# Performance work log

Measured on AMD Instinct MI355X. Metric: run time of the kernel, lower is better.

The kernel has to match this reference:

```python
import jax, jax.numpy as jnp
import numpy as np

D_MODEL = 512
D_PROJ = 32
N_CENT = 6
CORR_HIDDEN = max(D_MODEL // 16, 32)  # 32
LN_EPS = 1e-5
ALPHA_DIR = 5.0


def _layernorm(x, g, b):
    mu = x.mean(axis=-1, keepdims=True)
    var = jnp.mean((x - mu) ** 2, axis=-1, keepdims=True)
    return (x - mu) * jax.lax.rsqrt(var + LN_EPS) * g + b


def _l2norm(x, eps=1e-12):
    n = jnp.sqrt(jnp.sum(x * x, axis=-1, keepdims=True))
    return x / jnp.maximum(n, eps)


def setup_inputs() -> dict:
    key = jax.random.key(0)
    ks = jax.random.split(key, 8)
    B, N = 64, 1024
    x = jax.random.normal(ks[0], (B, N, D_MODEL), dtype=jnp.float32)
    s_in = 1.0 / np.sqrt(D_MODEL)
    proj_w = jax.random.uniform(ks[1], (D_PROJ, D_MODEL), jnp.float32, -s_in, s_in)
    proj_b = jax.random.uniform(ks[2], (D_PROJ,), jnp.float32, -s_in, s_in)
    ln_g = jnp.ones((D_PROJ,), jnp.float32)
    ln_b = jnp.zeros((D_PROJ,), jnp.float32)
    centroids = jax.random.uniform(ks[3], (N_CENT, D_PROJ), jnp.float32, -3.0, 3.0)
    s_c = 1.0 / np.sqrt(D_MODEL + D_PROJ)
    corr_in_w = jax.random.uniform(ks[4], (CORR_HIDDEN, D_MODEL + D_PROJ), jnp.float32, -s_c, s_c)
    corr_in_b = jax.random.uniform(ks[5], (CORR_HIDDEN,), jnp.float32, -s_c, s_c)
    # correction_out is zero-init in the module; use small random values so the
    # correction path is numerically exercised by the baseline.
    corr_out_w = jax.random.normal(ks[6], (D_MODEL, CORR_HIDDEN), jnp.float32) * 0.02
    corr_out_b = jax.random.normal(ks[7], (D_MODEL,), jnp.float32) * 0.02
    return {
        "x": x, "proj_w": proj_w, "proj_b": proj_b, "ln_g": ln_g, "ln_b": ln_b,
        "centroids": centroids,
        "corr_in_w": corr_in_w, "corr_in_b": corr_in_b,
        "corr_out_w": corr_out_w, "corr_out_b": corr_out_b,
        "gate_alpha": jnp.float32(0.0),
        "routing_log_temp": jnp.float32(1.6),
        "scale_evidence": jnp.float32(5.0),
    }


def reference(x, proj_w, proj_b, ln_g, ln_b, centroids, corr_in_w, corr_in_b,
              corr_out_w, corr_out_b, gate_alpha, routing_log_temp, scale_evidence):
    B, N, D = x.shape
    # per-variate RevIN-style normalization over the variate axis (dim=1), unbiased std
    rev_mean = x.mean(axis=1, keepdims=True)
    rev_var = jnp.sum((x - rev_mean) ** 2, axis=1, keepdims=True) / (N - 1)
    rev_std = jnp.sqrt(rev_var) + 1e-5
    x_norm = (x - rev_mean) / rev_std
    # geometric routing: proj -> LN -> cosine sim against centroids
    Q = _layernorm(jnp.einsum("bnd,pd->bnp", x_norm, proj_w) + proj_b, ln_g, ln_b)
    Q_n = _l2norm(Q)                      # [B,N,P]
    K_n = _l2norm(centroids)              # [K,P]
    sim_cos = jnp.einsum("bnp,kp->bnk", Q_n, K_n)
    soft_assign = jax.nn.softmax(sim_cos * jnp.exp(routing_log_temp), axis=-1)
    centroid_ctx = jnp.einsum("bnk,kp->bnp", soft_assign, centroids)
    # centroid-conditioned correction MLP (dropout is identity in eval)
    corr_input = jnp.concatenate([x_norm, centroid_ctx], axis=-1)  # [B,N,D+P]
    h = jax.nn.gelu(jnp.einsum("bnc,hc->bnh", corr_input, corr_in_w) + corr_in_b, approximate=False)
    correction = (jnp.einsum("bnh,dh->bnd", h, corr_out_w) + corr_out_b) * rev_std
    gate = jax.nn.sigmoid(gate_alpha)
    out = x + gate * correction
    # DST uncertainty (no-grad diagnostic)
    sim_ctrl = jax.lax.stop_gradient(sim_cos)
    dir_gate = jax.nn.softplus((sim_ctrl - sim_ctrl.mean(axis=-1, keepdims=True)) * ALPHA_DIR)
    s_ev = jax.nn.softplus(jax.lax.stop_gradient(scale_evidence))
    S_train = jnp.sum(dir_gate * s_ev + 1.0, axis=-1, keepdims=True)
    u_std = N_CENT / S_train
    # losses
    gram = K_n @ K_n.T
    ortho_loss = jnp.mean((gram - jnp.eye(N_CENT, dtype=x.dtype)) ** 2)
    avg_routing = soft_assign.mean(axis=(0, 1))
    latent_loss = jnp.mean((avg_routing - 1.0 / N_CENT) ** 2)
    return out, u_std, ortho_loss, latent_loss
```

## Files before the change

kernel.cpp:

```cpp
#include <hip/hip_runtime.h>
#include <cstdint>
#include <cstddef>

#define N_DIM 1024
#define D_DIM 512
#define M_DIM 65536
#define NC 6

typedef float f32x4 __attribute__((ext_vector_type(4)));
typedef __bf16 bf16x8 __attribute__((ext_vector_type(8)));

__device__ __forceinline__ float sp_f(float z) {
    return z > 20.f ? z : log1pf(expf(z));
}

__global__ void k_ortho(const float* __restrict__ cent, float* __restrict__ out_ortho) {
    __shared__ float skn[NC * 32];
    __shared__ float ssq[36];
    int t = threadIdx.x;
    if (t < NC) {
        float s = 0.f;
        for (int p = 0; p < 32; ++p) { float v = cent[t * 32 + p]; s += v * v; }
        float inv = 1.f / fmaxf(sqrtf(s), 1e-12f);
        for (int p = 0; p < 32; ++p) skn[t * 32 + p] = cent[t * 32 + p] * inv;
    }
    __syncthreads();
    if (t < 36) {
        int i = t / 6, j = t % 6;
        float g = 0.f;
        for (int p = 0; p < 32; ++p) g += skn[i * 32 + p] * skn[j * 32 + p];
        float d = g - (i == j ? 1.f : 0.f);
        ssq[t] = d * d;
    }
    __syncthreads();
    if (t == 0) {
        float s = 0.f;
        for (int i = 0; i < 36; ++i) s += ssq[i];
        *out_ortho = s / 36.f;
    }
}

__global__ void k_stat1(const float* __restrict__ x, float* __restrict__ part) {
    int bid = blockIdx.x;
    int b = bid >> 3, c = bid & 7;
    int d = threadIdx.x;
    const float* px = x + ((size_t)(b * N_DIM + c * 128)) * D_DIM + d;
    float s = 0.f, q = 0.f;
    for (int i = 0; i < 128; ++i) {
        float v = px[(size_t)i * D_DIM];
        s += v; q += v * v;
    }
    size_t o = ((size_t)bid * D_DIM + d) * 2;
    part[o] = s;
    part[o + 1] = q;
}

__global__ void k_stat2(const float* __restrict__ part, float* __restrict__ mean,
                        float* __restrict__ istd) {
    int b = blockIdx.x, d = threadIdx.x;
    float s = 0.f, q = 0.f;
    for (int c = 0; c < 8; ++c) {
        size_t o = (((size_t)(b * 8 + c)) * D_DIM + d) * 2;
        s += part[o]; q += part[o + 1];
    }
    float mu = s * (1.f / (float)N_DIM);
    float var = fmaxf((q - s * mu) * (1.f / (float)(N_DIM - 1)), 0.f);
    float sd = sqrtf(var) + 1e-5f;
    mean[b * D_DIM + d] = mu;
    istd[b * D_DIM + d] = 1.f / sd;
}

__launch_bounds__(256)
__global__ void mega(const float* __restrict__ x,
                     const float* __restrict__ pw, const float* __restrict__ proj_b,
                     const float* __restrict__ ln_g, const float* __restrict__ ln_b,
                     const float* __restrict__ cent,
                     const float* __restrict__ ciw, const float* __restrict__ cib,
                     const float* __restrict__ cow, const float* __restrict__ cob,
                     const float* __restrict__ ga, const float* __restrict__ rlt,
                     const float* __restrict__ sev,
                     const float* __restrict__ mean, const float* __restrict__ istd,
                     float* __restrict__ out, float* __restrict__ ustd_out,
                     float* __restrict__ acc_rout) {
    __shared__ float s_tile[4][16][65];
    __shared__ __align__(16) __bf16 s_h[4][16][40];
    __shared__ float s_asg[64][6];
    __shared__ float s_kn[192], s_cw[192];
    __shared__ float s_pb[32], s_g[32], s_bl[32], s_b2[32];
    __shared__ float s_scal[3];

    int tid = threadIdx.x;
    int wv = tid >> 6, ln = tid & 63;
    int l15 = ln & 15, lg = ln >> 4;

    if (tid < 192) {
        int k = tid >> 5, h = tid & 31;
        float s = 0.f;
        for (int p = 0; p < 32; ++p) s += cent[k * 32 + p] * ciw[h * 544 + 512 + p];
        s_cw[k * 32 + h] = s;
    }
    if (tid >= 192 && tid < 192 + NC) {
        int k = tid - 192;
        float s = 0.f;
        for (int p = 0; p < 32; ++p) { float v = cent[k * 32 + p]; s += v * v; }
        float inv = 1.f / fmaxf(sqrtf(s), 1e-12f);
        for (int p = 0; p < 32; ++p) s_kn[k * 32 + p] = cent[k * 32 + p] * inv;
    }
    if (tid == 198) {
        s_scal[0] = expf(rlt[0]);
        s_scal[1] = sp_f(sev[0]);
        s_scal[2] = 1.f / (1.f + expf(-ga[0]));
    }
    if (tid < 32) s_pb[tid] = proj_b[tid];
    else if (tid < 64) s_g[tid - 32] = ln_g[tid - 32];
    else if (tid < 96) s_bl[tid - 64] = ln_b[tid - 64];
    else if (tid < 128) s_b2[tid - 96] = cib[tid - 96];
    __syncthreads();

    int row0 = blockIdx.x * 64;
    int b = row0 >> 10;
    int wrow = row0 + wv * 16;
    int myrow = wrow + l15;

    const float* xr = x + (size_t)myrow * D_DIM;
    const float* mb = mean + b * D_DIM;
    const float* ib = istd + b * D_DIM;

    const float* wrow_[4];
    wrow_[0] = pw + (size_t)l15 * 512;
    wrow_[1] = pw + (size_t)(16 + l15) * 512;
    wrow_[2] = ciw + (size_t)l15 * 544;
    wrow_[3] = ciw + (size_t)(16 + l15) * 544;

    f32x4 acc[4];
    #pragma unroll
    for (int nf = 0; nf < 4; ++nf) acc[nf] = (f32x4){0.f, 0.f, 0.f, 0.f};

    for (int ks = 0; ks < 16; ++ks) {
        int k0 = ks * 32 + lg * 8;
        float4 xa = *(const float4*)(xr + k0);
        float4 xb = *(const float4*)(xr + k0 + 4);
        float4 ma = *(const float4*)(mb + k0);
        float4 m2 = *(const float4*)(mb + k0 + 4);
        float4 ia = *(const float4*)(ib + k0);
        float4 i2 = *(const float4*)(ib + k0 + 4);
        float xnf[8];
        xnf[0] = (xa.x - ma.x) * ia.x; xnf[1] = (xa.y - ma.y) * ia.y;
        xnf[2] = (xa.z - ma.z) * ia.z; xnf[3] = (xa.w - ma.w) * ia.w;
        xnf[4] = (xb.x - m2.x) * i2.x; xnf[5] = (xb.y - m2.y) * i2.y;
        xnf[6] = (xb.z - m2.z) * i2.z; xnf[7] = (xb.w - m2.w) * i2.w;
        bf16x8 ah, al;
        #pragma unroll
        for (int j = 0; j < 8; ++j) {
            __bf16 h = (__bf16)xnf[j];
            ah[j] = h;
            al[j] = (__bf16)(xnf[j] - (float)h);
        }
        #pragma unroll
        for (int nf = 0; nf < 4; ++nf) {
            float4 wa = *(const float4*)(wrow_[nf] + k0);
            float4 wb4 = *(const float4*)(wrow_[nf] + k0 + 4);
            float wf[8];
            wf[0] = wa.x; wf[1] = wa.y; wf[2] = wa.z; wf[3] = wa.w;
            wf[4] = wb4.x; wf[5] = wb4.y; wf[6] = wb4.z; wf[7] = wb4.w;
            bf16x8 wh;
            #pragma unroll
            for (int j = 0; j < 8; ++j) wh[j] = (__bf16)wf[j];
            acc[nf] = __builtin_amdgcn_mfma_f32_16x16x32_bf16(ah, wh, acc[nf], 0, 0, 0);
            if (nf < 2) {
                bf16x8 wl;
                #pragma unroll
                for (int j = 0; j < 8; ++j) wl[j] = (__bf16)(wf[j] - (float)wh[j]);
                acc[nf] = __builtin_amdgcn_mfma_f32_16x16x32_bf16(ah, wl, acc[nf], 0, 0, 0);
                acc[nf] = __builtin_amdgcn_mfma_f32_16x16x32_bf16(al, wh, acc[nf], 0, 0, 0);
            }
        }
    }
    #pragma unroll
    for (int nf = 0; nf < 4; ++nf)
        #pragma unroll
        for (int rg = 0; rg < 4; ++rg)
            s_tile[wv][lg * 4 + rg][nf * 16 + l15] = acc[nf][rg];
    __syncthreads();

    if (ln < 16) {
        int r = ln;
        int grow = wrow + r;
        const float* trow = &s_tile[wv][r][0];
        float P[32]; float mu = 0.f;
        #pragma unroll
        for (int p = 0; p < 32; ++p) { P[p] = trow[p] + s_pb[p]; mu += P[p]; }
        mu *= (1.f / 32.f);
        float var = 0.f;
        #pragma unroll
        for (int p = 0; p < 32; ++p) { float d = P[p] - mu; var += d * d; }
        var *= (1.f / 32.f);
        float rs = rsqrtf(var + 1e-5f);
        float q[32]; float n2 = 0.f;
        #pragma unroll
        for (int p = 0; p < 32; ++p) {
            q[p] = (P[p] - mu) * rs * s_g[p] + s_bl[p];
            n2 += q[p] * q[p];
        }
        float inv = 1.f / fmaxf(sqrtf(n2), 1e-12f);
        float sim[6];
        #pragma unroll
        for (int k = 0; k < 6; ++k) {
            float s = 0.f;
            #pragma unroll
            for (int p = 0; p < 32; ++p) s += q[p] * s_kn[k * 32 + p];
            sim[k] = s * inv;
        }
        float T = s_scal[0];
        float mx = sim[0];
        #pragma unroll
        for (int k = 1; k < 6; ++k) mx = fmaxf(mx, sim[k]);
        float e[6], es = 0.f;
        #pragma unroll
        for (int k = 0; k < 6; ++k) { e[k] = expf((sim[k] - mx) * T); es += e[k]; }
        float einv = 1.f / es;
        float a[6];
        #pragma unroll
        for (int k = 0; k < 6; ++k) { a[k] = e[k] * einv; s_asg[wv * 16 + r][k] = a[k]; }
        float msim = 0.f;
        #pragma unroll
        for (int k = 0; k < 6; ++k) msim += sim[k];
        msim *= (1.f / 6.f);
        float S = 6.f, sevv = s_scal[1];
        #pragma unroll
        for (int k = 0; k < 6; ++k) S += sevv * sp_f((sim[k] - msim) * 5.f);
        ustd_out[grow] = 6.f / S;
        #pragma unroll
        for (int h = 0; h < 32; ++h) {
            float v = trow[32 + h] + s_b2[h];
            #pragma unroll
            for (int k = 0; k < 6; ++k) v += a[k] * s_cw[k * 32 + h];
            float g = 0.5f * v * (1.f + erff(v * 0.70710678118654752f));
            s_h[wv][r][h] = (__bf16)g;
        }
    }
    __syncthreads();

    bf16x8 ha = *(const bf16x8*)&s_h[wv][l15][lg * 8];
    float gate = s_scal[2];
    for (int nf = 0; nf < 32; ++nf) {
        int col = nf * 16 + l15;
        float4 wa = *(const float4*)(cow + (size_t)col * 32 + lg * 8);
        float4 wb4 = *(const float4*)(cow + (size_t)col * 32 + lg * 8 + 4);
        bf16x8 wb;
        wb[0] = (__bf16)wa.x; wb[1] = (__bf16)wa.y; wb[2] = (__bf16)wa.z; wb[3] = (__bf16)wa.w;
        wb[4] = (__bf16)wb4.x; wb[5] = (__bf16)wb4.y; wb[6] = (__bf16)wb4.z; wb[7] = (__bf16)wb4.w;
        f32x4 z = (f32x4){0.f, 0.f, 0.f, 0.f};
        f32x4 d = __builtin_amdgcn_mfma_f32_16x16x32_bf16(ha, wb, z, 0, 0, 0);
        float bias = cob[col];
        float rsd = 1.f / ib[col];
        #pragma unroll
        for (int rg = 0; rg < 4; ++rg) {
            int row = wrow + lg * 4 + rg;
            float xv = x[(size_t)row * D_DIM + col];
            out[(size_t)row * D_DIM + col] = xv + gate * ((d[rg] + bias) * rsd);
        }
    }

    if (tid < 6) {
        float s = 0.f;
        for (int r = 0; r < 64; ++r) s += s_asg[r][tid];
        atomicAdd(acc_rout + tid, s);
    }
}

__global__ void k5(const float* __restrict__ acc, float* __restrict__ out_latent) {
    if (threadIdx.x == 0) {
        float s = 0.f;
        for (int k = 0; k < 6; ++k) {
            float av = acc[k] * (1.f / (float)M_DIM);
            float d = av - (1.f / 6.f);
            s += d * d;
        }
        *out_latent = s / 6.f;
    }
}

extern "C" void kernel_launch(void* const* d_in, const int* in_sizes, int n_in,
                              void* d_out, int out_size, void* d_ws, size_t ws_size,
                              hipStream_t stream) {
    const float* x      = (const float*)d_in[0];
    const float* proj_w = (const float*)d_in[1];
    const float* proj_b = (const float*)d_in[2];
    const float* ln_g   = (const float*)d_in[3];
    const float* ln_b   = (const float*)d_in[4];
    const float* cent   = (const float*)d_in[5];
    const float* ciw    = (const float*)d_in[6];
    const float* cib    = (const float*)d_in[7];
    const float* cow    = (const float*)d_in[8];
    const float* cob    = (const float*)d_in[9];
    const float* ga     = (const float*)d_in[10];
    const float* rlt    = (const float*)d_in[11];
    const float* sev    = (const float*)d_in[12];

    char* ws = (char*)d_ws;
    float* acc  = (float*)(ws + 0);
    float* mean = (float*)(ws + 1024);
    float* istd = (float*)(ws + 1024 + 131072);

    float* outp   = (float*)d_out;
    float* ustd   = outp + (size_t)M_DIM * D_DIM;
    float* ortho  = ustd + M_DIM;
    float* latent = ortho + 1;

    float* part = (float*)d_out;

    hipMemsetAsync(acc, 0, 6 * sizeof(float), stream);
    k_ortho<<<1, 64, 0, stream>>>(cent, ortho);
    k_stat1<<<512, 512, 0, stream>>>(x, part);
    k_stat2<<<64, 512, 0, stream>>>(part, mean, istd);
    mega<<<1024, 256, 0, stream>>>(x, proj_w, proj_b, ln_g, ln_b, cent, ciw, cib,
                                   cow, cob, ga, rlt, sev, mean, istd,
                                   outp, ustd, acc);
    k5<<<1, 64, 0, stream>>>(acc, latent);
}
```

Measured before the change: 174.3 us.

## Prepack weights to bf16 in a separate kernel and parallelize per-row epilogue

Adds a k_pack kernel that converts projection and correction weights to bf16 hi/lo splits once and precomputes normalized centroids, centroid-correction products and scalars, so the mega kernel no longer reconverts weights and recomputes these per block. The per-row LayerNorm/routing/GELU epilogue is spread across 4 lanes per row with shuffles instead of 16 lanes doing everything serially. The block barriers are dropped because each wave only touches its own smem slice. Routing sums go into 64 partial slots to reduce atomic contention, and a precomputed std replaces the per-column reciprocal. The cost is an extra kernel launch and more workspace traffic.

```diff
diff --git a/kernel.cpp b/kernel.cpp
--- a/kernel.cpp
+++ b/kernel.cpp
@@ -12,6 +12,45 @@
 
 __device__ __forceinline__ float sp_f(float z) {
     return z > 20.f ? z : log1pf(expf(z));
+}
+
+__global__ void k_pack(const float* __restrict__ pw, const float* __restrict__ ciw,
+                       const float* __restrict__ cow, const float* __restrict__ cent,
+                       const float* __restrict__ ga, const float* __restrict__ rlt,
+                       const float* __restrict__ sev,
+                       __bf16* __restrict__ bpa, __bf16* __restrict__ bpl,
+                       __bf16* __restrict__ w3p,
+                       float* __restrict__ kn, float* __restrict__ cw,
+                       float* __restrict__ scal) {
+    int bid = blockIdx.x, tid = threadIdx.x;
+    if (bid < 128) {
+        int i = bid * 256 + tid;
+        int c = i >> 9, k = i & 511;
+        float w = (c < 32) ? pw[c * 512 + k] : ciw[(c - 32) * 544 + k];
+        __bf16 hi = (__bf16)w;
+        bpa[i] = hi;
+        if (c < 32) bpl[i] = (__bf16)(w - (float)hi);
+    } else if (bid < 192) {
+        int j = (bid - 128) * 256 + tid;
+        w3p[j] = (__bf16)cow[j];
+    } else {
+        if (tid < 192) {
+            int k = tid >> 5, h = tid & 31;
+            float s = 0.f;
+            for (int p = 0; p < 32; ++p) s += cent[k * 32 + p] * ciw[h * 544 + 512 + p];
+            cw[k * 32 + h] = s;
+        } else if (tid < 192 + NC) {
+            int k = tid - 192;
+            float s = 0.f;
+            for (int p = 0; p < 32; ++p) { float v = cent[k * 32 + p]; s += v * v; }
+            float inv = 1.f / fmaxf(sqrtf(s), 1e-12f);
+            for (int p = 0; p < 32; ++p) kn[k * 32 + p] = cent[k * 32 + p] * inv;
+        } else if (tid == 198) {
+            scal[0] = expf(rlt[0]);
+            scal[1] = sp_f(sev[0]);
+            scal[2] = 1.f / (1.f + expf(-ga[0]));
+        }
+    }
 }
 
 __global__ void k_ortho(const float* __restrict__ cent, float* __restrict__ out_ortho) {
@@ -56,7 +95,7 @@
 }
 
 __global__ void k_stat2(const float* __restrict__ part, float* __restrict__ mean,
-                        float* __restrict__ istd) {
+                        float* __restrict__ istd, float* __restrict__ stdv) {
     int b = blockIdx.x, d = threadIdx.x;
     float s = 0.f, q = 0.f;
     for (int c = 0; c < 8; ++c) {
@@ -68,74 +107,46 @@
     float sd = sqrtf(var) + 1e-5f;
     mean[b * D_DIM + d] = mu;
     istd[b * D_DIM + d] = 1.f / sd;
+    stdv[b * D_DIM + d] = sd;
 }
 
 __launch_bounds__(256)
 __global__ void mega(const float* __restrict__ x,
-                     const float* __restrict__ pw, const float* __restrict__ proj_b,
-                     const float* __restrict__ ln_g, const float* __restrict__ ln_b,
-                     const float* __restrict__ cent,
-                     const float* __restrict__ ciw, const float* __restrict__ cib,
-                     const float* __restrict__ cow, const float* __restrict__ cob,
-                     const float* __restrict__ ga, const float* __restrict__ rlt,
-                     const float* __restrict__ sev,
+                     const float* __restrict__ proj_b, const float* __restrict__ ln_g,
+                     const float* __restrict__ ln_b, const float* __restrict__ cib,
+                     const float* __restrict__ cob,
                      const float* __restrict__ mean, const float* __restrict__ istd,
+                     const float* __restrict__ stdv,
+                     const float* __restrict__ kn, const float* __restrict__ cw,
+                     const float* __restrict__ scal,
+                     const __bf16* __restrict__ bpa, const __bf16* __restrict__ bpl,
+                     const __bf16* __restrict__ w3p,
                      float* __restrict__ out, float* __restrict__ ustd_out,
-                     float* __restrict__ acc_rout) {
-    __shared__ float s_tile[4][16][65];
+                     float* __restrict__ rout_part) {
+    __shared__ __align__(16) float s_tile[4][16][68];
     __shared__ __align__(16) __bf16 s_h[4][16][40];
-    __shared__ float s_asg[64][6];
-    __shared__ float s_kn[192], s_cw[192];
-    __shared__ float s_pb[32], s_g[32], s_bl[32], s_b2[32];
-    __shared__ float s_scal[3];
 
     int tid = threadIdx.x;
     int wv = tid >> 6, ln = tid & 63;
     int l15 = ln & 15, lg = ln >> 4;
 
-    if (tid < 192) {
-        int k = tid >> 5, h = tid & 31;
-        float s = 0.f;
-        for (int p = 0; p < 32; ++p) s += cent[k * 32 + p] * ciw[h * 544 + 512 + p];
-        s_cw[k * 32 + h] = s;
-    }
-    if (tid >= 192 && tid < 192 + NC) {
-        int k = tid - 192;
-        float s = 0.f;
-        for (int p = 0; p < 32; ++p) { float v = cent[k * 32 + p]; s += v * v; }
-        float inv = 1.f / fmaxf(sqrtf(s), 1e-12f);
-        for (int p = 0; p < 32; ++p) s_kn[k * 32 + p] = cent[k * 32 + p] * inv;
-    }
-    if (tid == 198) {
-        s_scal[0] = expf(rlt[0]);
-        s_scal[1] = sp_f(sev[0]);
-        s_scal[2] = 1.f / (1.f + expf(-ga[0]));
-    }
-    if (tid < 32) s_pb[tid] = proj_b[tid];
-    else if (tid < 64) s_g[tid - 32] = ln_g[tid - 32];
-    else if (tid < 96) s_bl[tid - 64] = ln_b[tid - 64];
-    else if (tid < 128) s_b2[tid - 96] = cib[tid - 96];
-    __syncthreads();
-
     int row0 = blockIdx.x * 64;
     int b = row0 >> 10;
     int wrow = row0 + wv * 16;
-    int myrow = wrow + l15;
-
-    const float* xr = x + (size_t)myrow * D_DIM;
+
+    const float* xr = x + (size_t)(wrow + l15) * D_DIM;
     const float* mb = mean + b * D_DIM;
     const float* ib = istd + b * D_DIM;
 
-    const float* wrow_[4];
-    wrow_[0] = pw + (size_t)l15 * 512;
-    wrow_[1] = pw + (size_t)(16 + l15) * 512;
-    wrow_[2] = ciw + (size_t)l15 * 544;
-    wrow_[3] = ciw + (size_t)(16 + l15) * 544;
-
-    f32x4 acc[4];
-    #pragma unroll
-    for (int nf = 0; nf < 4; ++nf) acc[nf] = (f32x4){0.f, 0.f, 0.f, 0.f};
-
+    const __bf16* w0 = bpa + (size_t)l15 * 512;
+    const __bf16* w1 = bpa + (size_t)(16 + l15) * 512;
+    const __bf16* w2 = bpa + (size_t)(32 + l15) * 512;
+    const __bf16* w3 = bpa + (size_t)(48 + l15) * 512;
+    const __bf16* wl0 = bpl + (size_t)l15 * 512;
+    const __bf16* wl1 = bpl + (size_t)(16 + l15) * 512;
+
+    f32x4 a0 = {0.f, 0.f, 0.f, 0.f}, a1 = a0, a2 = a0, a3 = a0;
+    #pragma unroll 4
     for (int ks = 0; ks < 16; ++ks) {
         int k0 = ks * 32 + lg * 8;
         float4 xa = *(const float4*)(xr + k0);
@@ -156,62 +167,71 @@
             ah[j] = h;
             al[j] = (__bf16)(xnf[j] - (float)h);
         }
-        #pragma unroll
-        for (int nf = 0; nf < 4; ++nf) {
-            float4 wa = *(const float4*)(wrow_[nf] + k0);
-            float4 wb4 = *(const float4*)(wrow_[nf] + k0 + 4);
-            float wf[8];
-            wf[0] = wa.x; wf[1] = wa.y; wf[2] = wa.z; wf[3] = wa.w;
-            wf[4] = wb4.x; wf[5] = wb4.y; wf[6] = wb4.z; wf[7] = wb4.w;
-            bf16x8 wh;
-            #pragma unroll
-            for (int j = 0; j < 8; ++j) wh[j] = (__bf16)wf[j];
-            acc[nf] = __builtin_amdgcn_mfma_f32_16x16x32_bf16(ah, wh, acc[nf], 0, 0, 0);
-            if (nf < 2) {
-                bf16x8 wl;
-                #pragma unroll
-                for (int j = 0; j < 8; ++j) wl[j] = (__bf16)(wf[j] - (float)wh[j]);
-                acc[nf] = __builtin_amdgcn_mfma_f32_16x16x32_bf16(ah, wl, acc[nf], 0, 0, 0);
-                acc[nf] = __builtin_amdgcn_mfma_f32_16x16x32_bf16(al, wh, acc[nf], 0, 0, 0);
-            }
-        }
+        bf16x8 wh0 = *(const bf16x8*)(w0 + k0);
+        bf16x8 wh1 = *(const bf16x8*)(w1 + k0);
+        a0 = __builtin_amdgcn_mfma_f32_16x16x32_bf16(ah, wh0, a0, 0, 0, 0);
+        a0 = __builtin_amdgcn_mfma_f32_16x16x32_bf16(ah, *(const bf16x8*)(wl0 + k0), a0, 0, 0, 0);
+        a0 = __builtin_amdgcn_mfma_f32_16x16x32_bf16(al, wh0, a0, 0, 0, 0);
+        a1 = __builtin_amdgcn_mfma_f32_16x16x32_bf16(ah, wh1, a1, 0, 0, 0);
+        a1 = __builtin_amdgcn_mfma_f32_16x16x32_bf16(ah, *(const bf16x8*)(wl1 + k0), a1, 0, 0, 0);
+        a1 = __builtin_amdgcn_mfma_f32_16x16x32_bf16(al, wh1, a1, 0, 0, 0);
+        a2 = __builtin_amdgcn_mfma_f32_16x16x32_bf16(ah, *(const bf16x8*)(w2 + k0), a2, 0, 0, 0);
+        a3 = __builtin_amdgcn_mfma_f32_16x16x32_bf16(ah, *(const bf16x8*)(w3 + k0), a3, 0, 0, 0);
     }
     #pragma unroll
-    for (int nf = 0; nf < 4; ++nf)
-        #pragma unroll
-        for (int rg = 0; rg < 4; ++rg)
-            s_tile[wv][lg * 4 + rg][nf * 16 + l15] = acc[nf][rg];
-    __syncthreads();
-
-    if (ln < 16) {
-        int r = ln;
-        int grow = wrow + r;
-        const float* trow = &s_tile[wv][r][0];
-        float P[32]; float mu = 0.f;
-        #pragma unroll
-        for (int p = 0; p < 32; ++p) { P[p] = trow[p] + s_pb[p]; mu += P[p]; }
-        mu *= (1.f / 32.f);
-        float var = 0.f;
-        #pragma unroll
-        for (int p = 0; p < 32; ++p) { float d = P[p] - mu; var += d * d; }
-        var *= (1.f / 32.f);
-        float rs = rsqrtf(var + 1e-5f);
-        float q[32]; float n2 = 0.f;
-        #pragma unroll
-        for (int p = 0; p < 32; ++p) {
-            q[p] = (P[p] - mu) * rs * s_g[p] + s_bl[p];
-            n2 += q[p] * q[p];
-        }
+    for (int rg = 0; rg < 4; ++rg) {
+        s_tile[wv][lg * 4 + rg][l15]      = a0[rg];
+        s_tile[wv][lg * 4 + rg][16 + l15] = a1[rg];
+        s_tile[wv][lg * 4 + rg][32 + l15] = a2[rg];
+        s_tile[wv][lg * 4 + rg][48 + l15] = a3[rg];
+    }
+
+    {
+        int r = ln >> 2, sub = ln & 3;
+        const float* tr = &s_tile[wv][r][0];
+        float4 t0 = *(const float4*)(tr + sub * 8);
+        float4 t1 = *(const float4*)(tr + sub * 8 + 4);
+        float4 pb0 = *(const float4*)(proj_b + sub * 8);
+        float4 pb1 = *(const float4*)(proj_b + sub * 8 + 4);
+        float P[8];
+        P[0] = t0.x + pb0.x; P[1] = t0.y + pb0.y; P[2] = t0.z + pb0.z; P[3] = t0.w + pb0.w;
+        P[4] = t1.x + pb1.x; P[5] = t1.y + pb1.y; P[6] = t1.z + pb1.z; P[7] = t1.w + pb1.w;
+        float m = 0.f;
+        #pragma unroll
+        for (int j = 0; j < 8; ++j) m += P[j];
+        m += __shfl_xor(m, 1); m += __shfl_xor(m, 2);
+        float mu = m * (1.f / 32.f);
+        float v = 0.f;
+        #pragma unroll
+        for (int j = 0; j < 8; ++j) { float d = P[j] - mu; v += d * d; }
+        v += __shfl_xor(v, 1); v += __shfl_xor(v, 2);
+        float rs = rsqrtf(v * (1.f / 32.f) + 1e-5f);
+        float4 g0 = *(const float4*)(ln_g + sub * 8);
+        float4 g1 = *(const float4*)(ln_g + sub * 8 + 4);
+        float4 bl0 = *(const float4*)(ln_b + sub * 8);
+        float4 bl1 = *(const float4*)(ln_b + sub * 8 + 4);
+        float gg[8] = {g0.x, g0.y, g0.z, g0.w, g1.x, g1.y, g1.z, g1.w};
+        float bb[8] = {bl0.x, bl0.y, bl0.z, bl0.w, bl1.x, bl1.y, bl1.z, bl1.w};
+        float q[8]; float n2 = 0.f;
+        #pragma unroll
+        for (int j = 0; j < 8; ++j) {
+            q[j] = (P[j] - mu) * rs * gg[j] + bb[j];
+            n2 += q[j] * q[j];
+        }
+        n2 += __shfl_xor(n2, 1); n2 += __shfl_xor(n2, 2);
         float inv = 1.f / fmaxf(sqrtf(n2), 1e-12f);
         float sim[6];
         #pragma unroll
         for (int k = 0; k < 6; ++k) {
-            float s = 0.f;
-            #pragma unroll
-            for (int p = 0; p < 32; ++p) s += q[p] * s_kn[k * 32 + p];
+            const float* kr = kn + k * 32 + sub * 8;
+            float4 ka = *(const float4*)(kr);
+            float4 kb = *(const float4*)(kr + 4);
+            float s = q[0] * ka.x + q[1] * ka.y + q[2] * ka.z + q[3] * ka.w
+                    + q[4] * kb.x + q[5] * kb.y + q[6] * kb.z + q[7] * kb.w;
+            s += __shfl_xor(s, 1); s += __shfl_xor(s, 2);
             sim[k] = s * inv;
         }
-        float T = s_scal[0];
+        float T = scal[0], sevv = scal[1];
         float mx = sim[0];
         #pragma unroll
         for (int k = 1; k < 6; ++k) mx = fmaxf(mx, sim[k]);
@@ -221,61 +241,77 @@
         float einv = 1.f / es;
         float a[6];
         #pragma unroll
-        for (int k = 0; k < 6; ++k) { a[k] = e[k] * einv; s_asg[wv * 16 + r][k] = a[k]; }
+        for (int k = 0; k < 6; ++k) a[k] = e[k] * einv;
         float msim = 0.f;
         #pragma unroll
         for (int k = 0; k < 6; ++k) msim += sim[k];
         msim *= (1.f / 6.f);
-        float S = 6.f, sevv = s_scal[1];
+        float S = 6.f;
         #pragma unroll
         for (int k = 0; k < 6; ++k) S += sevv * sp_f((sim[k] - msim) * 5.f);
-        ustd_out[grow] = 6.f / S;
-        #pragma unroll
-        for (int h = 0; h < 32; ++h) {
-            float v = trow[32 + h] + s_b2[h];
-            #pragma unroll
-            for (int k = 0; k < 6; ++k) v += a[k] * s_cw[k * 32 + h];
-            float g = 0.5f * v * (1.f + erff(v * 0.70710678118654752f));
-            s_h[wv][r][h] = (__bf16)g;
-        }
-    }
-    __syncthreads();
-
-    bf16x8 ha = *(const bf16x8*)&s_h[wv][l15][lg * 8];
-    float gate = s_scal[2];
+        if (sub == 0) ustd_out[wrow + r] = 6.f / S;
+        float4 h0 = *(const float4*)(tr + 32 + sub * 8);
+        float4 h1 = *(const float4*)(tr + 32 + sub * 8 + 4);
+        float4 c0 = *(const float4*)(cib + sub * 8);
+        float4 c1 = *(const float4*)(cib + sub * 8 + 4);
+        float vh[8] = {h0.x + c0.x, h0.y + c0.y, h0.z + c0.z, h0.w + c0.w,
+                       h1.x + c1.x, h1.y + c1.y, h1.z + c1.z, h1.w + c1.w};
+        #pragma unroll
+        for (int k = 0; k < 6; ++k) {
+            const float* cr = cw + k * 32 + sub * 8;
+            float4 ca = *(const float4*)(cr);
+            float4 cb = *(const float4*)(cr + 4);
+            vh[0] += a[k] * ca.x; vh[1] += a[k] * ca.y; vh[2] += a[k] * ca.z; vh[3] += a[k] * ca.w;
+            vh[4] += a[k] * cb.x; vh[5] += a[k] * cb.y; vh[6] += a[k] * cb.z; vh[7] += a[k] * cb.w;
+        }
+        bf16x8 hv;
+        #pragma unroll
+        for (int j = 0; j < 8; ++j) {
+            float gv = 0.5f * vh[j] * (1.f + erff(vh[j] * 0.70710678118654752f));
+            hv[j] = (__bf16)gv;
+        }
+        *(bf16x8*)(&s_h[wv][r][sub * 8]) = hv;
+        #pragma unroll
+        for (int k = 0; k < 6; ++k) {
+            float rv = (sub == 0) ? a[k] : 0.f;
+            rv += __shfl_xor(rv, 4); rv += __shfl_xor(rv, 8);
+            rv += __shfl_xor(rv, 16); rv += __shfl_xor(rv, 32);
+            if (ln == 0) atomicAdd(rout_part + (blockIdx.x & 63) * 6 + k, rv);
+        }
+    }
+
+    bf16x8 ha = *(const bf16x8*)(&s_h[wv][l15][lg * 8]);
+    float gate = scal[2];
+    const float* sb = stdv + b * D_DIM;
     for (int nf = 0; nf < 32; ++nf) {
         int col = nf * 16 + l15;
-        float4 wa = *(const float4*)(cow + (size_t)col * 32 + lg * 8);
-        float4 wb4 = *(const float4*)(cow + (size_t)col * 32 + lg * 8 + 4);
-        bf16x8 wb;
-        wb[0] = (__bf16)wa.x; wb[1] = (__bf16)wa.y; wb[2] = (__bf16)wa.z; wb[3] = (__bf16)wa.w;
-        wb[4] = (__bf16)wb4.x; wb[5] = (__bf16)wb4.y; wb[6] = (__bf16)wb4.z; wb[7] = (__bf16)wb4.w;
-        f32x4 z = (f32x4){0.f, 0.f, 0.f, 0.f};
+        bf16x8 wb = *(const bf16x8*)(w3p + col * 32 + lg * 8);
+        f32x4 z = {0.f, 0.f, 0.f, 0.f};
         f32x4 d = __builtin_amdgcn_mfma_f32_16x16x32_bf16(ha, wb, z, 0, 0, 0);
         float bias = cob[col];
-        float rsd = 1.f / ib[col];
+        float rsd = sb[col];
         #pragma unroll
         for (int rg = 0; rg < 4; ++rg) {
-            int row = wrow + lg * 4 + rg;
-            float xv = x[(size_t)row * D_DIM + col];
-            out[(size_t)row * D_DIM + col] = xv + gate * ((d[rg] + bias) * rsd);
-        }
-    }
-
-    if (tid < 6) {
+            size_t idx = (size_t)(wrow + lg * 4 + rg) * D_DIM + col;
+            out[idx] = x[idx] + gate * ((d[rg] + bias) * rsd);
+        }
+    }
+}
+
+__global__ void k5(const float* __restrict__ rp, float* __restrict__ out_latent) {
+    __shared__ float sv[6];
+    int t = threadIdx.x;
+    if (t < 6) {
         float s = 0.f;
-        for (int r = 0; r < 64; ++r) s += s_asg[r][tid];
-        atomicAdd(acc_rout + tid, s);
-    }
-}
-
-__global__ void k5(const float* __restrict__ acc, float* __restrict__ out_latent) {
-    if (threadIdx.x == 0) {
+        for (int i = 0; i < 64; ++i) s += rp[i * 6 + t];
+        sv[t] = s;
+    }
+    __syncthreads();
+    if (t == 0) {
         float s = 0.f;
         for (int k = 0; k < 6; ++k) {
-            float av = acc[k] * (1.f / (float)M_DIM);
-            float d = av - (1.f / 6.f);
-            s += d * d;
+            float av = sv[k] * (1.f / (float)M_DIM) - (1.f / 6.f);
+            s += av * av;
         }
         *out_latent = s / 6.f;
     }
@@ -299,9 +335,16 @@
     const float* sev    = (const float*)d_in[12];
 
     char* ws = (char*)d_ws;
-    float* acc  = (float*)(ws + 0);
-    float* mean = (float*)(ws + 1024);
-    float* istd = (float*)(ws + 1024 + 131072);
+    float*  rout = (float*)(ws + 0);
+    float*  kn   = (float*)(ws + 2048);
+    float*  cwv  = (float*)(ws + 4096);
+    float*  scal = (float*)(ws + 6144);
+    __bf16* bpa  = (__bf16*)(ws + 8192);
+    __bf16* bpl  = (__bf16*)(ws + 73728);
+    __bf16* w3p  = (__bf16*)(ws + 106496);
+    float*  mean = (float*)(ws + 139264);
+    float*  istd = (float*)(ws + 270336);
+    float*  stdv = (float*)(ws + 401408);
 
     float* outp   = (float*)d_out;
     float* ustd   = outp + (size_t)M_DIM * D_DIM;
@@ -310,12 +353,14 @@
 
     float* part = (float*)d_out;
 
-    hipMemsetAsync(acc, 0, 6 * sizeof(float), stream);
+    hipMemsetAsync(rout, 0, 64 * 6 * sizeof(float), stream);
+    k_pack<<<193, 256, 0, stream>>>(proj_w, ciw, cow, cent, ga, rlt, sev,
+                                    bpa, bpl, w3p, kn, cwv, scal);
     k_ortho<<<1, 64, 0, stream>>>(cent, ortho);
     k_stat1<<<512, 512, 0, stream>>>(x, part);
-    k_stat2<<<64, 512, 0, stream>>>(part, mean, istd);
-    mega<<<1024, 256, 0, stream>>>(x, proj_w, proj_b, ln_g, ln_b, cent, ciw, cib,
-                                   cow, cob, ga, rlt, sev, mean, istd,
-                                   outp, ustd, acc);
-    k5<<<1, 64, 0, stream>>>(acc, latent);
-}
+    k_stat2<<<64, 512, 0, stream>>>(part, mean, istd, stdv);
+    mega<<<1024, 256, 0, stream>>>(x, proj_b, ln_g, ln_b, cib, cob,
+                                   mean, istd, stdv, kn, cwv, scal,
+                                   bpa, bpl, w3p, outp, ustd, rout);
+    k5<<<1, 64, 0, stream>>>(rout, latent);
+}
```

Result: faster. 146.0 us (-16.2%).
